# Performance work log

Hardware: AMD Instinct MI355X
Metric: run time of the kernel (lower is better)

Reference implementation:

```python
import jax, jax.numpy as jnp
import numpy as np

N = 2048          # nodes
IN_DIM = 512      # in_dim
H = 8             # num_heads
HD = IN_DIM // H  # head_dim = 64
L = 5             # max_path_len
E = 32768         # edges
D_EDGE = 64       # edge_feat_dim


def setup_inputs() -> dict:
    key = jax.random.key(0)
    ks = jax.random.split(key, 14)
    w = 1.0 / np.sqrt(IN_DIM)
    return {
        "node_feat": jax.random.normal(ks[0], (N, IN_DIM), jnp.float32),
        "edge_index": jax.random.randint(ks[1], (2, E), 0, N, dtype=jnp.int32),
        "max_path_len": 5,
        "shortest_distances": jax.random.randint(ks[2], (N, N), 0, L + 1, dtype=jnp.int32),
        "shortest_paths": jax.random.randint(ks[3], (N, N, L), 0, E + 1, dtype=jnp.int32),  # E == padding row
        "edge_feat": jax.random.normal(ks[4], (E, D_EDGE), jnp.float32),
        "attention_mask": jnp.zeros((N, N), jnp.int32),
        "WQ": jax.random.normal(ks[5], (IN_DIM, IN_DIM), jnp.float32) * w,
        "bQ": jax.random.normal(ks[6], (IN_DIM,), jnp.float32) * 0.02,
        "WK": jax.random.normal(ks[7], (IN_DIM, IN_DIM), jnp.float32) * w,
        "bK": jax.random.normal(ks[8], (IN_DIM,), jnp.float32) * 0.02,
        "WV": jax.random.normal(ks[9], (IN_DIM, IN_DIM), jnp.float32) * w,
        "bV": jax.random.normal(ks[10], (IN_DIM,), jnp.float32) * 0.02,
        "WO": jax.random.normal(ks[11], (IN_DIM, IN_DIM), jnp.float32) * w,
        "bO": jnp.zeros((IN_DIM,), jnp.float32),
        "spatial_bias": jax.random.normal(ks[12], ((L + 1) * H, 1), jnp.float32) * 0.02,
        "edge_weight": jax.random.normal(ks[13], ((L + 1) * H, D_EDGE), jnp.float32) * 0.02,
    }


def reference(node_feat, edge_index, max_path_len, shortest_distances, shortest_paths,
              edge_feat, attention_mask, WQ, bQ, WK, bK, WV, bV, WO, bO,
              spatial_bias, edge_weight):
    Nn, D = node_feat.shape
    Lp = max_path_len  # min(max_path_len, max_shortest_path_len); distances reach Lp here

    Q = (node_feat @ WQ + bQ).reshape(Nn, H, HD)
    K = (node_feat @ WK + bK).reshape(Nn, H, HD)
    V = (node_feat @ WV + bV).reshape(Nn, H, HD)

    # QK^T / sqrt(head_dim), laid out [N, N, H] as in the original after permute
    scores = jnp.einsum('nhd,mhd->nmh', Q, K) / np.sqrt(HD).astype(np.float32)

    # SpatialEncoding: bias table [(L+1)*H, 1] -> [L+1, H]; gather by clamped distance
    sp_table = spatial_bias.reshape(Lp + 1, H)
    dist = jnp.clip(shortest_distances, 0, Lp)
    scores = scores + sp_table[dist]  # [N, N, H]

    # EdgeEncoding: einsum('xyld,ldh->xyh') refactored as per-edge projection then gather
    W_e = edge_weight[: Lp * H].reshape(Lp, H, D_EDGE)  # (reshape[L,H,D].permute -> [L,D,H])
    padded = jnp.concatenate([edge_feat, jnp.zeros((1, D_EDGE), edge_feat.dtype)], axis=0)
    T = jnp.einsum('ed,lhd->elh', padded, W_e)  # [E+1, L, H]
    sp = shortest_paths[:, :, :Lp]
    gathered = T[sp, jnp.arange(Lp)[None, None, :]]  # [N, N, L, H]
    scores = scores + gathered.sum(axis=2)

    mask = attention_mask.astype(bool)
    scores = jnp.where(mask[:, :, None], -jnp.inf, scores)

    # NOTE: original applies softmax over dim=-1 of the [N, N, H] tensor (the head axis);
    # faithfully reproduced here. Dropout is identity (eval / p for inference).
    attn = jax.nn.softmax(scores, axis=-1)

    out = jnp.einsum('nmh,mhd->nhd', attn, V).reshape(Nn, D)
    return out @ WO + bO
```

## Files before the change

kernel.cpp:

```cpp
#include <hip/hip_runtime.h>

#define NN     2048
#define DIM    512
#define NH     8
#define HD     64
#define NE     32768
#define EPAD   32832
#define CHUNKS 8
#define CHSZ   (NN/CHUNKS)
#define NJT    (CHSZ/64)
#define QBLK   32
#define LOG2E  1.4426950408889634f

typedef __attribute__((ext_vector_type(8))) short bf16x8;
typedef __attribute__((ext_vector_type(4))) float f32x4;
typedef __attribute__((ext_vector_type(4))) unsigned int u32x4;

#define MFMA(a,b,c) __builtin_amdgcn_mfma_f32_16x16x32_bf16((a),(b),(c),0,0,0)

__device__ __forceinline__ float bf2f(unsigned int u16){
  union { unsigned int i; float f; } v; v.i = u16 << 16; return v.f;
}
__device__ __forceinline__ unsigned short f2bf(float f){
  union { float ff; unsigned int i; } v; v.ff = f;
  return (unsigned short)((v.i + 0x7fffu + ((v.i >> 16) & 1u)) >> 16);
}

__global__ __launch_bounds__(256) void prep_k(
    const float* __restrict__ X, const float* __restrict__ ef, const float* __restrict__ ew,
    unsigned short* __restrict__ Xb, unsigned short* __restrict__ pEF, unsigned short* __restrict__ pEW,
    const float* __restrict__ a0, const float* __restrict__ a1,
    const float* __restrict__ a2, const float* __restrict__ a3,
    unsigned short* __restrict__ Wt)
{
  __shared__ unsigned short tile[32][33];
  if (blockIdx.x < 1540){
    long g = (long)blockIdx.x*256 + threadIdx.x;
    const long GX = (long)NN*DIM/8;
    const long GE = (long)EPAD*8;
    const float* src; unsigned short* dst; long off, lim8;
    if (g < GX){ src = X;  dst = Xb;  off = g;        lim8 = GX; }
    else if (g < GX+GE){ src = ef; dst = pEF; off = g-GX; lim8 = (long)NE*8; }
    else { off = g-GX-GE; if (off >= 512) return; src = ew; dst = pEW; lim8 = 320; }
    unsigned short o[8];
    if (off < lim8){
      #pragma unroll
      for (int i=0;i<8;i++) o[i] = f2bf(src[off*8+i]);
    } else {
      #pragma unroll
      for (int i=0;i<8;i++) o[i] = 0;
    }
    *(uint4*)(dst + off*8) = *(const uint4*)o;
  } else {
    int b2 = blockIdx.x - 1540;
    int bz = b2 >> 8, rem = b2 & 255;
    int bx = (rem & 15)*32, by = (rem >> 4)*32;
    int tx = threadIdx.x & 31, ty = threadIdx.x >> 5;
    const float* src = bz==0 ? a0 : bz==1 ? a1 : bz==2 ? a2 : a3;
    unsigned short* dst = Wt + (size_t)bz*DIM*DIM;
    #pragma unroll
    for (int i=0;i<32;i+=8) tile[ty+i][tx] = f2bf(src[(size_t)(by+ty+i)*DIM + bx+tx]);
    __syncthreads();
    #pragma unroll
    for (int i=0;i<32;i+=8) dst[(size_t)(bx+ty+i)*DIM + by+tx] = tile[tx][ty+i];
  }
}

__global__ __launch_bounds__(256) void gemm_bt(
    const unsigned short* __restrict__ A1, const unsigned short* __restrict__ A2,
    const float* __restrict__ bias, unsigned short* __restrict__ C, float* __restrict__ Cf,
    int M, int N, int K, int bias_row)
{
  int lane = threadIdx.x & 63, w = threadIdx.x >> 6;
  int quad = lane >> 4, low = lane & 15;
  int m0 = blockIdx.y*64 + w*16;
  int n0 = blockIdx.x*32;
  f32x4 acc[2];
  acc[0] = (f32x4){0.f,0.f,0.f,0.f};
  acc[1] = (f32x4){0.f,0.f,0.f,0.f};
  #pragma unroll 4
  for (int k0=0; k0<K; k0+=32){
    bf16x8 a = *(const bf16x8*)(A1 + (size_t)(m0+low)*K + k0 + quad*8);
    #pragma unroll
    for (int t=0;t<2;t++){
      bf16x8 b = *(const bf16x8*)(A2 + (size_t)(n0+16*t+low)*K + k0 + quad*8);
      acc[t] = MFMA(a, b, acc[t]);
    }
  }
  #pragma unroll
  for (int t=0;t<2;t++){
    #pragma unroll
    for (int r=0;r<4;r++){
      int row = m0 + quad*4 + r;
      int col = n0 + 16*t + low;
      float v = acc[t][r];
      if (bias) v += bias[bias_row ? row : col];
      if (Cf) Cf[(size_t)row*N + col] = v;
      else    C [(size_t)row*N + col] = f2bf(v);
    }
  }
}

__global__ __launch_bounds__(256) void gemm_t2(
    const unsigned short* __restrict__ A1, const unsigned short* __restrict__ A2,
    unsigned short* __restrict__ T2L)
{
  int lane = threadIdx.x & 63, w = threadIdx.x >> 6;
  int quad = lane >> 4, low = lane & 15;
  int m0 = blockIdx.y*64 + w*16;
  int n0 = blockIdx.x*32;
  f32x4 acc[2];
  acc[0] = (f32x4){0.f,0.f,0.f,0.f};
  acc[1] = (f32x4){0.f,0.f,0.f,0.f};
  #pragma unroll
  for (int k0=0; k0<64; k0+=32){
    bf16x8 a = *(const bf16x8*)(A1 + (size_t)(m0+low)*64 + k0 + quad*8);
    #pragma unroll
    for (int t=0;t<2;t++){
      bf16x8 b = *(const bf16x8*)(A2 + (size_t)(n0+16*t+low)*64 + k0 + quad*8);
      acc[t] = MFMA(a, b, acc[t]);
    }
  }
  #pragma unroll
  for (int t=0;t<2;t++){
    #pragma unroll
    for (int r=0;r<4;r++){
      int row = m0 + quad*4 + r;
      int col = n0 + 16*t + low;
      T2L[((size_t)(col>>3)*EPAD + row)*8 + (col&7)] = f2bf(acc[t][r]);
    }
  }
}

__global__ __launch_bounds__(256) void biasqkv_k(
    const unsigned short* __restrict__ T2L, const float* __restrict__ spb,
    const int* __restrict__ dist, const int* __restrict__ sp, const int* __restrict__ maskp,
    unsigned short* __restrict__ biasB,
    const unsigned short* __restrict__ Xb, const unsigned short* __restrict__ Wt,
    const float* __restrict__ bQ, const float* __restrict__ bK, const float* __restrict__ bV,
    unsigned short* __restrict__ Qb, unsigned short* __restrict__ Kb, unsigned short* __restrict__ Vtb)
{
  __shared__ float sptab[48];
  if (blockIdx.x >= 512){
    if (threadIdx.x < 48) sptab[threadIdx.x] = spb[threadIdx.x];
    __syncthreads();
    long pix = (long)(blockIdx.x - 512)*256 + threadIdx.x;
    int dd = __builtin_nontemporal_load(dist + pix);
    int mk = __builtin_nontemporal_load(maskp + pix);
    int e[5];
    #pragma unroll
    for (int l=0;l<5;l++) e[l] = __builtin_nontemporal_load(sp + pix*5 + l);
    dd = dd < 0 ? 0 : (dd > 5 ? 5 : dd);
    float b[8];
    #pragma unroll
    for (int x=0;x<8;x++) b[x] = sptab[dd*8 + x];
    #pragma unroll
    for (int l=0;l<5;l++){
      int ee = e[l];
      if ((unsigned)ee > (unsigned)NE) ee = NE;
      uint4 tv = *(const uint4*)(T2L + ((size_t)l*EPAD + ee)*8);
      b[0] += bf2f(tv.x & 0xffffu); b[1] += bf2f(tv.x >> 16);
      b[2] += bf2f(tv.y & 0xffffu); b[3] += bf2f(tv.y >> 16);
      b[4] += bf2f(tv.z & 0xffffu); b[5] += bf2f(tv.z >> 16);
      b[6] += bf2f(tv.w & 0xffffu); b[7] += bf2f(tv.w >> 16);
    }
    unsigned short o[8];
    #pragma unroll
    for (int x=0;x<8;x++) o[x] = mk ? f2bf(-1e30f) : f2bf(b[x]);
    *(uint4*)(biasB + pix*8) = *(const uint4*)o;
  } else {
    int bid = blockIdx.x;
    int lane = threadIdx.x & 63, w = threadIdx.x >> 6;
    int quad = lane >> 4, low = lane & 15;
    int m0 = (bid >> 4)*64 + w*16;
    int n0 = (bid & 15)*32;
    f32x4 acc[3][2];
    #pragma unroll
    for (int z=0;z<3;z++){ acc[z][0]=(f32x4){0.f,0.f,0.f,0.f}; acc[z][1]=(f32x4){0.f,0.f,0.f,0.f}; }
    #pragma unroll 2
    for (int k0=0; k0<DIM; k0+=32){
      bf16x8 a = *(const bf16x8*)(Xb + (size_t)(m0+low)*DIM + k0 + quad*8);
      #pragma unroll
      for (int z=0;z<3;z++){
        #pragma unroll
        for (int t=0;t<2;t++){
          bf16x8 b = *(const bf16x8*)(Wt + (size_t)z*DIM*DIM + (size_t)(n0+16*t+low)*DIM + k0 + quad*8);
          acc[z][t] = MFMA(a, b, acc[z][t]);
        }
      }
    }
    #pragma unroll
    for (int t=0;t<2;t++){
      #pragma unroll
      for (int r=0;r<4;r++){
        int row = m0 + quad*4 + r;
        int col = n0 + 16*t + low;
        Qb[(size_t)row*DIM + col] = f2bf(acc[0][t][r] + bQ[col]);
        Kb[(size_t)row*DIM + col] = f2bf(acc[1][t][r] + bK[col]);
        Vtb[(size_t)col*NN + row] = f2bf(acc[2][t][r] + bV[col]);
      }
    }
  }
}

__global__ __launch_bounds__(512, 4) void attn_k(
    const unsigned short* __restrict__ Qb, const unsigned short* __restrict__ Kb,
    const unsigned short* __restrict__ Vt, const unsigned short* __restrict__ biasB,
    float* __restrict__ partO)
{
  __shared__ __attribute__((aligned(16))) float sld[NH][QBLK][68];
  int tid = threadIdx.x;
  int lane = tid & 63, h = tid >> 6;
  int quad = lane >> 4, low = lane & 15;
  int q0 = blockIdx.x * QBLK;
  int chunk = blockIdx.y;

  bf16x8 aq[2][2];
  #pragma unroll
  for (int sq=0;sq<2;sq++)
    #pragma unroll
    for (int s=0;s<2;s++)
      aq[sq][s] = *(const bf16x8*)(Qb + (size_t)(q0+sq*16+low)*DIM + h*HD + s*32 + quad*8);

  f32x4 accO[2][4];
  #pragma unroll
  for (int sq=0;sq<2;sq++)
    #pragma unroll
    for (int t=0;t<4;t++) accO[sq][t] = (f32x4){0.f,0.f,0.f,0.f};

  uint4 pb[4];
  #pragma unroll
  for (int it=0; it<4; ++it){
    int p = tid + it*512;
    int qq = p >> 6, mm = p & 63;
    pb[it] = *(const uint4*)(biasB + ((size_t)(q0+qq)*NN + chunk*CHSZ + mm)*8);
  }

  for (int jt=0; jt<NJT; ++jt){
    int m0 = chunk*CHSZ + jt*64;
    __syncthreads();

    #pragma unroll
    for (int it=0; it<4; ++it){
      int p = tid + it*512;
      int qq = p >> 6, mm = p & 63;
      uint4 tv = pb[it];
      sld[0][qq][mm] = bf2f(tv.x & 0xffffu); sld[1][qq][mm] = bf2f(tv.x >> 16);
      sld[2][qq][mm] = bf2f(tv.y & 0xffffu); sld[3][qq][mm] = bf2f(tv.y >> 16);
      sld[4][qq][mm] = bf2f(tv.z & 0xffffu); sld[5][qq][mm] = bf2f(tv.z >> 16);
      sld[6][qq][mm] = bf2f(tv.w & 0xffffu); sld[7][qq][mm] = bf2f(tv.w >> 16);
    }
    if (jt+1 < NJT){
      #pragma unroll
      for (int it=0; it<4; ++it){
        int p = tid + it*512;
        int qq = p >> 6, mm = p & 63;
        pb[it] = *(const uint4*)(biasB + ((size_t)(q0+qq)*NN + m0 + 64 + mm)*8);
      }
    }
    __syncthreads();

    f32x4 S[2][4];
    #pragma unroll
    for (int sq=0;sq<2;sq++)
      #pragma unroll
      for (int t=0;t<4;t++) S[sq][t] = (f32x4){0.f,0.f,0.f,0.f};
    #pragma unroll
    for (int s=0;s<2;s++){
      #pragma unroll
      for (int t=0;t<4;t++){
        bf16x8 bk = *(const bf16x8*)(Kb + (size_t)(m0+16*t+low)*DIM + h*HD + s*32 + quad*8);
        #pragma unroll
        for (int sq=0;sq<2;sq++)
          S[sq][t] = MFMA(aq[sq][s], bk, S[sq][t]);
      }
    }
    #pragma unroll
    for (int sq=0;sq<2;sq++){
      #pragma unroll
      for (int t=0;t<4;t++){
        #pragma unroll
        for (int r=0;r<4;r++){
          float* slot = &sld[h][sq*16+quad*4+r][low+16*t];
          *slot = S[sq][t][r]*0.125f + *slot;
        }
      }
    }
    __syncthreads();

    #pragma unroll
    for (int it=0; it<4; ++it){
      int p = tid + it*512;
      int qq = p >> 6, mm = p & 63;
      float s0[8];
      #pragma unroll
      for (int x=0;x<8;x++) s0[x] = sld[x][qq][mm];
      float mx = s0[0];
      #pragma unroll
      for (int x=1;x<8;x++) mx = fmaxf(mx, s0[x]);
      float sum = 0.f;
      #pragma unroll
      for (int x=0;x<8;x++){ s0[x] = exp2f((s0[x]-mx)*LOG2E); sum += s0[x]; }
      float inv = (mx < -1e29f) ? 0.f : 1.f/sum;
      #pragma unroll
      for (int x=0;x<8;x++) sld[x][qq][mm] = s0[x]*inv;
    }
    __syncthreads();

    bf16x8 ap[2][2];
    #pragma unroll
    for (int sq=0;sq<2;sq++){
      #pragma unroll
      for (int s=0;s<2;s++){
        const float* pp = &sld[h][sq*16+low][s*32 + quad*8];
        float4 x0 = *(const float4*)pp;
        float4 x1 = *(const float4*)(pp + 4);
        bf16x8 a;
        a[0]=(short)f2bf(x0.x); a[1]=(short)f2bf(x0.y); a[2]=(short)f2bf(x0.z); a[3]=(short)f2bf(x0.w);
        a[4]=(short)f2bf(x1.x); a[5]=(short)f2bf(x1.y); a[6]=(short)f2bf(x1.z); a[7]=(short)f2bf(x1.w);
        ap[sq][s] = a;
      }
    }
    #pragma unroll
    for (int s=0;s<2;s++){
      #pragma unroll
      for (int t=0;t<4;t++){
        bf16x8 bv = *(const bf16x8*)(Vt + (size_t)(h*HD + 16*t + low)*NN + m0 + s*32 + quad*8);
        #pragma unroll
        for (int sq=0;sq<2;sq++)
          accO[sq][t] = MFMA(ap[sq][s], bv, accO[sq][t]);
      }
    }
  }

  #pragma unroll
  for (int sq=0;sq<2;sq++){
    #pragma unroll
    for (int t=0;t<4;t++){
      #pragma unroll
      for (int r=0;r<4;r++){
        int q = sq*16 + quad*4 + r;
        partO[(((size_t)chunk*NN + q0 + q)*NH + h)*HD + 16*t + low] = accO[sq][t][r];
      }
    }
  }
}

__global__ __launch_bounds__(512) void merge_k(const float* __restrict__ partO,
                                               unsigned short* __restrict__ Obf)
{
  size_t idx = (size_t)blockIdx.x*512 + threadIdx.x;
  float s = 0.f;
  #pragma unroll
  for (int c=0;c<CHUNKS;c++) s += partO[(size_t)c*NN*DIM + idx];
  Obf[idx] = f2bf(s);
}

extern "C" void kernel_launch(void* const* d_in, const int* in_sizes, int n_in,
                              void* d_out, int out_size, void* d_ws, size_t ws_size,
                              hipStream_t stream)
{
  const float* X    = (const float*)d_in[0];
  const int*  dist  = (const int*)d_in[3];
  const int*  sp    = (const int*)d_in[4];
  const float* ef   = (const float*)d_in[5];
  const int*  maskp = (const int*)d_in[6];
  const float* WQ   = (const float*)d_in[7];
  const float* bQ   = (const float*)d_in[8];
  const float* WK   = (const float*)d_in[9];
  const float* bK   = (const float*)d_in[10];
  const float* WV   = (const float*)d_in[11];
  const float* bV   = (const float*)d_in[12];
  const float* WO   = (const float*)d_in[13];
  const float* bO   = (const float*)d_in[14];
  const float* spb  = (const float*)d_in[15];
  const float* ew   = (const float*)d_in[16];

  char* ws = (char*)d_ws;
  unsigned short* Wt   = (unsigned short*)(ws + 0);
  unsigned short* Xb   = (unsigned short*)(ws + 2097152);
  unsigned short* Qb   = (unsigned short*)(ws + 4194304);
  unsigned short* Kb   = (unsigned short*)(ws + 6291456);
  unsigned short* Vtb  = (unsigned short*)(ws + 8388608);
  unsigned short* pEF  = (unsigned short*)(ws + 10485760);
  unsigned short* pEW  = (unsigned short*)(ws + 14688256);
  unsigned short* T2L  = (unsigned short*)(ws + 14696448);
  unsigned short* Obf  = (unsigned short*)(ws + 18898944);
  unsigned short* biasB= (unsigned short*)(ws + 20996096);
  float*          pO   = (float*)(ws + 88104960);

  prep_k<<<dim3(2564), dim3(256), 0, stream>>>(X, ef, ew, Xb, pEF, pEW, WQ, WK, WV, WO, Wt);
  gemm_t2<<<dim3(2,513), dim3(256), 0, stream>>>(pEF, pEW, T2L);
  biasqkv_k<<<dim3(512 + NN*NN/256), dim3(256), 0, stream>>>(
      T2L, spb, dist, sp, maskp, biasB, Xb, Wt, bQ, bK, bV, Qb, Kb, Vtb);
  attn_k<<<dim3(NN/QBLK, CHUNKS), dim3(512), 0, stream>>>(Qb, Kb, Vtb, biasB, pO);
  merge_k<<<dim3(2048), dim3(512), 0, stream>>>(pO, Obf);
  gemm_bt<<<dim3(16,32), dim3(256), 0, stream>>>(Obf, Wt + 786432, bO, (unsigned short*)nullptr, (float*)d_out, NN, DIM, DIM, 0);
}
```

Baseline: 371.6 us.

## Fuse bias add into softmax pass and pack probabilities as bf16 pairs in LDS

The attention kernel no longer scatters the bias tile into shared memory in a separate pass. Bias stays in registers and is added while the softmax reads the QK scores, which removes one LDS write phase and one barrier per tile. Softmax output is now stored as packed bf16 pairs (two heads per 32-bit word) and unpacked for the PV MFMA, halving LDS traffic for the probabilities. The next-tile bias prefetch moves after the softmax, and the bias-gather kernel's table loads become nontemporal.

Measured after the change: 583.3 us. 1.57x slower.

```diff
diff --git a/kernel.cpp b/kernel.cpp
--- a/kernel.cpp
+++ b/kernel.cpp
@@ -158,11 +158,11 @@
     for (int l=0;l<5;l++){
       int ee = e[l];
       if ((unsigned)ee > (unsigned)NE) ee = NE;
-      uint4 tv = *(const uint4*)(T2L + ((size_t)l*EPAD + ee)*8);
-      b[0] += bf2f(tv.x & 0xffffu); b[1] += bf2f(tv.x >> 16);
-      b[2] += bf2f(tv.y & 0xffffu); b[3] += bf2f(tv.y >> 16);
-      b[4] += bf2f(tv.z & 0xffffu); b[5] += bf2f(tv.z >> 16);
-      b[6] += bf2f(tv.w & 0xffffu); b[7] += bf2f(tv.w >> 16);
+      u32x4 tv = __builtin_nontemporal_load((const u32x4*)(T2L + ((size_t)l*EPAD + ee)*8));
+      b[0] += bf2f(tv[0] & 0xffffu); b[1] += bf2f(tv[0] >> 16);
+      b[2] += bf2f(tv[1] & 0xffffu); b[3] += bf2f(tv[1] >> 16);
+      b[4] += bf2f(tv[2] & 0xffffu); b[5] += bf2f(tv[2] >> 16);
+      b[6] += bf2f(tv[3] & 0xffffu); b[7] += bf2f(tv[3] >> 16);
     }
     unsigned short o[8];
     #pragma unroll
@@ -209,6 +209,7 @@
     float* __restrict__ partO)
 {
   __shared__ __attribute__((aligned(16))) float sld[NH][QBLK][68];
+  unsigned int* p2 = (unsigned int*)sld;
   int tid = threadIdx.x;
   int lane = tid & 63, h = tid >> 6;
   int quad = lane >> 4, low = lane & 15;
@@ -238,27 +239,6 @@
 
   for (int jt=0; jt<NJT; ++jt){
     int m0 = chunk*CHSZ + jt*64;
-    __syncthreads();
-
-    #pragma unroll
-    for (int it=0; it<4; ++it){
-      int p = tid + it*512;
-      int qq = p >> 6, mm = p & 63;
-      uint4 tv = pb[it];
-      sld[0][qq][mm] = bf2f(tv.x & 0xffffu); sld[1][qq][mm] = bf2f(tv.x >> 16);
-      sld[2][qq][mm] = bf2f(tv.y & 0xffffu); sld[3][qq][mm] = bf2f(tv.y >> 16);
-      sld[4][qq][mm] = bf2f(tv.z & 0xffffu); sld[5][qq][mm] = bf2f(tv.z >> 16);
-      sld[6][qq][mm] = bf2f(tv.w & 0xffffu); sld[7][qq][mm] = bf2f(tv.w >> 16);
-    }
-    if (jt+1 < NJT){
-      #pragma unroll
-      for (int it=0; it<4; ++it){
-        int p = tid + it*512;
-        int qq = p >> 6, mm = p & 63;
-        pb[it] = *(const uint4*)(biasB + ((size_t)(q0+qq)*NN + m0 + 64 + mm)*8);
-      }
-    }
-    __syncthreads();
 
     f32x4 S[2][4];
     #pragma unroll
@@ -275,15 +255,15 @@
           S[sq][t] = MFMA(aq[sq][s], bk, S[sq][t]);
       }
     }
+    __syncthreads();
+
     #pragma unroll
     for (int sq=0;sq<2;sq++){
       #pragma unroll
       for (int t=0;t<4;t++){
         #pragma unroll
-        for (int r=0;r<4;r++){
-          float* slot = &sld[h][sq*16+quad*4+r][low+16*t];
-          *slot = S[sq][t][r]*0.125f + *slot;
-        }
+        for (int r=0;r<4;r++)
+          sld[h][sq*16+quad*4+r][low+16*t] = S[sq][t][r]*0.125f;
       }
     }
     __syncthreads();
@@ -292,9 +272,16 @@
     for (int it=0; it<4; ++it){
       int p = tid + it*512;
       int qq = p >> 6, mm = p & 63;
+      uint4 tv = pb[it];
       float s0[8];
-      #pragma unroll
-      for (int x=0;x<8;x++) s0[x] = sld[x][qq][mm];
+      s0[0] = sld[0][qq][mm] + bf2f(tv.x & 0xffffu);
+      s0[1] = sld[1][qq][mm] + bf2f(tv.x >> 16);
+      s0[2] = sld[2][qq][mm] + bf2f(tv.y & 0xffffu);
+      s0[3] = sld[3][qq][mm] + bf2f(tv.y >> 16);
+      s0[4] = sld[4][qq][mm] + bf2f(tv.z & 0xffffu);
+      s0[5] = sld[5][qq][mm] + bf2f(tv.z >> 16);
+      s0[6] = sld[6][qq][mm] + bf2f(tv.w & 0xffffu);
+      s0[7] = sld[7][qq][mm] + bf2f(tv.w >> 16);
       float mx = s0[0];
       #pragma unroll
       for (int x=1;x<8;x++) mx = fmaxf(mx, s0[x]);
@@ -303,7 +290,19 @@
       for (int x=0;x<8;x++){ s0[x] = exp2f((s0[x]-mx)*LOG2E); sum += s0[x]; }
       float inv = (mx < -1e29f) ? 0.f : 1.f/sum;
       #pragma unroll
-      for (int x=0;x<8;x++) sld[x][qq][mm] = s0[x]*inv;
+      for (int pr=0;pr<4;pr++){
+        unsigned int u = (unsigned int)f2bf(s0[2*pr]*inv)
+                       | ((unsigned int)f2bf(s0[2*pr+1]*inv) << 16);
+        p2[pr*2176 + qq*68 + mm] = u;
+      }
+    }
+    if (jt+1 < NJT){
+      #pragma unroll
+      for (int it=0; it<4; ++it){
+        int p = tid + it*512;
+        int qq = p >> 6, mm = p & 63;
+        pb[it] = *(const uint4*)(biasB + ((size_t)(q0+qq)*NN + m0 + 64 + mm)*8);
+      }
     }
     __syncthreads();
 
@@ -312,12 +311,16 @@
     for (int sq=0;sq<2;sq++){
       #pragma unroll
       for (int s=0;s<2;s++){
-        const float* pp = &sld[h][sq*16+low][s*32 + quad*8];
-        float4 x0 = *(const float4*)pp;
-        float4 x1 = *(const float4*)(pp + 4);
+        const uint4* pp = (const uint4*)(p2 + (h>>1)*2176 + (size_t)(sq*16+low)*68 + s*32 + quad*8);
+        uint4 w0 = pp[0], w1 = pp[1];
         bf16x8 a;
-        a[0]=(short)f2bf(x0.x); a[1]=(short)f2bf(x0.y); a[2]=(short)f2bf(x0.z); a[3]=(short)f2bf(x0.w);
-        a[4]=(short)f2bf(x1.x); a[5]=(short)f2bf(x1.y); a[6]=(short)f2bf(x1.z); a[7]=(short)f2bf(x1.w);
+        if (h & 1){
+          a[0]=(short)(w0.x>>16); a[1]=(short)(w0.y>>16); a[2]=(short)(w0.z>>16); a[3]=(short)(w0.w>>16);
+          a[4]=(short)(w1.x>>16); a[5]=(short)(w1.y>>16); a[6]=(short)(w1.z>>16); a[7]=(short)(w1.w>>16);
+        } else {
+          a[0]=(short)(w0.x&0xffffu); a[1]=(short)(w0.y&0xffffu); a[2]=(short)(w0.z&0xffffu); a[3]=(short)(w0.w&0xffffu);
+          a[4]=(short)(w1.x&0xffffu); a[5]=(short)(w1.y&0xffffu); a[6]=(short)(w1.z&0xffffu); a[7]=(short)(w1.w&0xffffu);
+        }
         ap[sq][s] = a;
       }
     }
```
